# Optimization experiments

Hardware: AMD Instinct MI355X
Metric: run time of the kernel (lower is better)

## Reference

```python
import jax, jax.numpy as jnp
import numpy as np

ALPHA = 0.2  # LeakyReLU negative slope
NEG_INF = -9e15


def setup_inputs() -> dict:
    key = jax.random.key(0)
    ks = jax.random.split(key, 6)
    B, N, F_in, F_out = 16, 1024, 1024, 512
    x = jax.random.normal(ks[0], (B, N, F_in), dtype=jnp.float32)
    adj = jax.random.randint(ks[1], (B, N, N), 0, 2, dtype=jnp.int32)
    W = jax.random.normal(ks[2], (F_in, F_out), dtype=jnp.float32) * 0.02
    a = jax.random.normal(ks[3], (2 * F_out, 1), dtype=jnp.float32) * 0.02
    fc_w = jax.random.normal(ks[4], (F_out, 2 * F_out), dtype=jnp.float32) * 0.02
    fc_b = jnp.zeros((F_out,), dtype=jnp.float32)
    return {"x": x, "adj": adj, "W": W, "a": a, "fc_w": fc_w, "fc_b": fc_b}


def reference(x, adj, W, a, fc_w, fc_b):
    # h: [B, N, F_out]
    h = jnp.matmul(x, W)
    F_out = W.shape[1]
    # The original builds a_input = concat(h_i, h_j) of shape [B,N,N,2F] and
    # contracts with a. Equivalently (same math, no O(N^2 F) intermediate):
    # e_ij = leakyrelu(h_i . a[:F] + h_j . a[F:])
    a1 = a[:F_out, 0]  # [F_out]
    a2 = a[F_out:, 0]  # [F_out]
    f1 = jnp.einsum('bnf,f->bn', h, a1)  # source term
    f2 = jnp.einsum('bnf,f->bn', h, a2)  # target term
    e = jax.nn.leaky_relu(f1[:, :, None] + f2[:, None, :], negative_slope=ALPHA)  # [B,N,N]
    attention = jnp.where(adj > 0, e, jnp.full_like(e, NEG_INF))
    attention = jax.nn.softmax(attention, axis=2)
    # dropout is identity in eval mode
    agg = jnp.matmul(attention, h)  # [B,N,F_out]
    h_prime = jnp.concatenate([agg, h], axis=2)  # [B,N,2F]
    h_prime = jnp.matmul(h_prime, fc_w.T) + fc_b
    return jax.nn.elu(h_prime)  # concat=True path
```

## Files before the change

### kernel.cpp

```cpp
#include <hip/hip_runtime.h>

#define ALPHA 0.2f

typedef __attribute__((ext_vector_type(8))) short short8;
typedef __attribute__((ext_vector_type(4))) float f32x4;

__device__ __forceinline__ unsigned short f2b(float f) {
  unsigned int u; __builtin_memcpy(&u, &f, 4);
  unsigned int r = (u + 0x7FFFu + ((u >> 16) & 1u)) >> 16;
  return (unsigned short)r;
}
__device__ __forceinline__ float b2f(unsigned short v) {
  unsigned int u = ((unsigned int)v) << 16; float f; __builtin_memcpy(&f, &u, 4); return f;
}
__device__ __forceinline__ void gl_lds16(const unsigned short* g, unsigned short* l) {
  __builtin_amdgcn_global_load_lds((__attribute__((address_space(1))) void*)g,
                                   (__attribute__((address_space(3))) void*)l, 16, 0, 0);
}
__device__ __forceinline__ uint4 pack8(float4 v0, float4 v1) {
  alignas(16) unsigned short o[8];
  o[0] = f2b(v0.x); o[1] = f2b(v0.y); o[2] = f2b(v0.z); o[3] = f2b(v0.w);
  o[4] = f2b(v1.x); o[5] = f2b(v1.y); o[6] = f2b(v1.z); o[7] = f2b(v1.w);
  return *(const uint4*)o;
}

__device__ __forceinline__ void cvt_f4(const float* __restrict__ in,
                                       unsigned short* __restrict__ out,
                                       unsigned int f4idx) {
  float4 v = ((const float4*)in)[f4idx];
  alignas(8) unsigned short o[4];
  o[0] = f2b(v.x); o[1] = f2b(v.y); o[2] = f2b(v.z); o[3] = f2b(v.w);
  ((uint2*)out)[f4idx] = *(const uint2*)o;
}

__global__ __launch_bounds__(256) void prep1(const float* __restrict__ fcw,
                                             unsigned short* __restrict__ fcwb,
                                             const float* __restrict__ W,
                                             unsigned short* __restrict__ Wt,
                                             float* __restrict__ f1z,
                                             float* __restrict__ f2z) {
  __shared__ alignas(16) unsigned short tile[64][72];
  unsigned int bx = blockIdx.x;
  unsigned int tid = threadIdx.x;
  if (bx < 256u) {
    unsigned int base = bx * 512u;
    cvt_f4(fcw, fcwb, base + tid);
    cvt_f4(fcw, fcwb, base + 256u + tid);
  } else if (bx < 384u) {
    unsigned int idx = bx - 256u;
    unsigned int k0 = (idx >> 3) * 64, n0 = (idx & 7) * 64;
    #pragma unroll
    for (int p = 0; p < 4; p++) {
      int r = p * 16 + (tid >> 4);
      int c = (tid & 15) * 4;
      float4 v = *(const float4*)(W + (size_t)(k0 + r) * 512 + n0 + c);
      tile[r][c] = f2b(v.x); tile[r][c + 1] = f2b(v.y);
      tile[r][c + 2] = f2b(v.z); tile[r][c + 3] = f2b(v.w);
    }
    __syncthreads();
    int f = tid >> 2;
    int ic = (tid & 3) * 16;
    alignas(16) unsigned short buf[16];
    #pragma unroll
    for (int k = 0; k < 16; k++) buf[k] = tile[ic + k][f];
    uint4* dst = (uint4*)(Wt + (size_t)(n0 + f) * 1024 + k0 + ic);
    dst[0] = ((const uint4*)buf)[0];
    dst[1] = ((const uint4*)buf)[1];
  } else {
    float4 z = {0.f, 0.f, 0.f, 0.f};
    #pragma unroll
    for (int i = 0; i < 16; i++) ((float4*)f1z)[i * 256 + tid] = z;
    #pragma unroll
    for (int i = 0; i < 16; i++) ((float4*)f2z)[i * 256 + tid] = z;
  }
}

__global__ __launch_bounds__(256) void rowsum_P(const int* __restrict__ adj,
                                                const float* __restrict__ f1,
                                                const float* __restrict__ f2,
                                                float* __restrict__ invl,
                                                unsigned short* __restrict__ P) {
  int row = blockIdx.x * 4 + (threadIdx.x >> 6);
  int lane = threadIdx.x & 63;
  int b = row >> 10;
  float f1v = f1[row];
  const int4* ap = (const int4*)(adj + (size_t)row * 1024) + lane * 4;
  int4 a0 = ap[0];
  int4 a1 = ap[1];
  int4 a2 = ap[2];
  int4 a3 = ap[3];
  int av[16] = {a0.x, a0.y, a0.z, a0.w, a1.x, a1.y, a1.z, a1.w,
                a2.x, a2.y, a2.z, a2.w, a3.x, a3.y, a3.z, a3.w};
  const float* f2p = f2 + (b << 10) + lane * 16;
  float4 v0 = ((const float4*)f2p)[0];
  float4 v1 = ((const float4*)f2p)[1];
  float4 v2 = ((const float4*)f2p)[2];
  float4 v3 = ((const float4*)f2p)[3];
  float fv[16] = {v0.x, v0.y, v0.z, v0.w, v1.x, v1.y, v1.z, v1.w,
                  v2.x, v2.y, v2.z, v2.w, v3.x, v3.y, v3.z, v3.w};
  float s = 0.f;
  alignas(16) unsigned short o[16];
  #pragma unroll
  for (int j = 0; j < 16; j++) {
    float p = 0.f;
    if (av[j] > 0) {
      float z = f1v + fv[j];
      z = z > 0.f ? z : ALPHA * z;
      p = __expf(z);
      s += p;
    }
    o[j] = f2b(p);
  }
  uint4* dst = (uint4*)(P + (size_t)row * 1024 + lane * 16);
  dst[0] = ((const uint4*)o)[0];
  dst[1] = ((const uint4*)o)[1];
  #pragma unroll
  for (int off = 32; off > 0; off >>= 1) s += __shfl_down(s, off);
  if (lane == 0) invl[row] = 1.0f / s;
}

template <int EPI, int CVTA>
__global__ __launch_bounds__(512, 4) void gemm_bt(
    const void* __restrict__ A_, size_t aBS,
    const unsigned short* __restrict__ Bt, size_t bBS,
    int K,
    void* __restrict__ outp, size_t oBS, int ldo, int ocol,
    const float* __restrict__ scale,
    const float* __restrict__ bias,
    unsigned short* __restrict__ htout,
    float* __restrict__ f1g, float* __restrict__ f2g) {
  __shared__ alignas(16) unsigned short smem[32768];
  unsigned short* As = smem;
  unsigned short* Bs = smem + 16384;
  const int tid = threadIdx.x;
  const int lane = tid & 63;
  const int w = tid >> 6;
  const int m0 = blockIdx.x * 128;
  const int n0 = blockIdx.y * 128;
  const int zb = blockIdx.z;
  const unsigned short* Btb = Bt + (size_t)zb * bBS;

  f32x4 acc[4][2];
  #pragma unroll
  for (int i = 0; i < 4; i++)
    #pragma unroll
    for (int j = 0; j < 2; j++)
      #pragma unroll
      for (int r = 0; r < 4; r++) acc[i][j][r] = 0.f;

  const int lr = lane >> 3;
  const int lc = (lane & 7) ^ lr;
  const unsigned short* ag = nullptr;
  const float* agf = nullptr;
  if (CVTA)
    agf = (const float*)A_ + (size_t)(m0 + w * 8 + lr) * K + lc * 8;
  else
    ag = (const unsigned short*)A_ + (size_t)zb * aBS + (size_t)(m0 + w * 8 + lr) * K + lc * 8;
  const unsigned short* bg = Btb + (size_t)(n0 + w * 8 + lr) * K + lc * 8;
  const int sb0 = (w * 8) * 64;
  const int sb1 = (64 + w * 8) * 64;
  const int lofs = lane * 8;

  const int wm = (w & 1) * 64;
  const int wn = (w >> 1) * 32;
  const int row16 = lane & 15;
  const int quad = lane >> 4;
  const int sw = row16 & 7;

  if (CVTA) {
    float4 av[2][2];
    #pragma unroll
    for (int t = 0; t < 2; t++) {
      av[t][0] = *(const float4*)(agf + (size_t)(t * 64) * K);
      av[t][1] = *(const float4*)(agf + (size_t)(t * 64) * K + 4);
    }
    gl_lds16(bg, Bs + sb0);
    gl_lds16(bg + (size_t)64 * K, Bs + sb1);
    *(uint4*)(As + sb0 + lofs) = pack8(av[0][0], av[0][1]);
    *(uint4*)(As + sb1 + lofs) = pack8(av[1][0], av[1][1]);
  } else {
    gl_lds16(ag, As + sb0);
    gl_lds16(ag + (size_t)64 * K, As + sb1);
    gl_lds16(bg, Bs + sb0);
    gl_lds16(bg + (size_t)64 * K, Bs + sb1);
  }
  __syncthreads();

  int bufo = 0;
  for (int k0 = 0; k0 < K; k0 += 64) {
    const int nbufo = bufo ^ 8192;
    const bool pf = (k0 + 64 < K);
    float4 av[2][2];
    if (pf) {
      if (CVTA) {
        #pragma unroll
        for (int t = 0; t < 2; t++) {
          av[t][0] = *(const float4*)(agf + (k0 + 64) + (size_t)(t * 64) * K);
          av[t][1] = *(const float4*)(agf + (k0 + 64) + (size_t)(t * 64) * K + 4);
        }
      } else {
        gl_lds16(ag + (k0 + 64), As + nbufo + sb0);
        gl_lds16(ag + (k0 + 64) + (size_t)64 * K, As + nbufo + sb1);
      }
      gl_lds16(bg + (k0 + 64), Bs + nbufo + sb0);
      gl_lds16(bg + (k0 + 64) + (size_t)64 * K, Bs + nbufo + sb1);
    }
    short8 af[2][4], bf[2][2];
    #pragma unroll
    for (int s = 0; s < 2; s++) {
      #pragma unroll
      for (int i = 0; i < 4; i++)
        af[s][i] = *(const short8*)(As + bufo + (wm + i * 16 + row16) * 64 + ((s * 4 + quad) ^ sw) * 8);
      #pragma unroll
      for (int j = 0; j < 2; j++)
        bf[s][j] = *(const short8*)(Bs + bufo + (wn + j * 16 + row16) * 64 + ((s * 4 + quad) ^ sw) * 8);
    }
    #pragma unroll
    for (int s = 0; s < 2; s++)
      #pragma unroll
      for (int am = 0; am < 4; am++)
        #pragma unroll
        for (int bn = 0; bn < 2; bn++)
          acc[am][bn] = __builtin_amdgcn_mfma_f32_16x16x32_bf16(af[s][am], bf[s][bn], acc[am][bn], 0, 0, 0);
    if (pf && CVTA) {
      *(uint4*)(As + nbufo + sb0 + lofs) = pack8(av[0][0], av[0][1]);
      *(uint4*)(As + nbufo + sb1 + lofs) = pack8(av[1][0], av[1][1]);
    }
    __syncthreads();
    bufo = nbufo;
  }

  const int col = lane & 15;
  const int r0 = quad * 4;
  #pragma unroll
  for (int am = 0; am < 4; am++) {
    #pragma unroll
    for (int bn = 0; bn < 2; bn++) {
      #pragma unroll
      for (int r = 0; r < 4; r++) {
        int m = m0 + wm + am * 16 + r0 + r;
        int n = n0 + wn + bn * 16 + col;
        float v = acc[am][bn][r];
        if (EPI == 3) v *= scale[zb * 1024 + m];
        if (EPI == 2) {
          v += bias[n];
          v = v > 0.f ? v : expm1f(v);
          ((float*)outp)[(size_t)m * ldo + n] = v;
        } else {
          ((unsigned short*)outp)[(size_t)zb * oBS + (size_t)m * ldo + ocol + n] = f2b(v);
        }
      }
    }
  }

  if (EPI == 1) {
    float* fbuf = (float*)smem;
    if (tid < 256) fbuf[tid] = 0.f;
    __syncthreads();
    float a1v[2], a2v[2];
    #pragma unroll
    for (int bn = 0; bn < 2; bn++) {
      int n = n0 + wn + bn * 16 + col;
      a1v[bn] = scale[n];
      a2v[bn] = scale[512 + n];
    }
    float p1[16], p2[16];
    #pragma unroll
    for (int am = 0; am < 4; am++)
      #pragma unroll
      for (int r = 0; r < 4; r++) {
        float s1 = 0.f, s2 = 0.f;
        #pragma unroll
        for (int bn = 0; bn < 2; bn++) {
          float hb = b2f(f2b(acc[am][bn][r]));
          s1 += hb * a1v[bn];
          s2 += hb * a2v[bn];
        }
        p1[am * 4 + r] = s1;
        p2[am * 4 + r] = s2;
      }
    #pragma unroll
    for (int mask = 1; mask < 16; mask <<= 1)
      #pragma unroll
      for (int e = 0; e < 16; e++) {
        p1[e] += __shfl_xor(p1[e], mask);
        p2[e] += __shfl_xor(p2[e], mask);
      }
    if ((lane & 15) == 0) {
      #pragma unroll
      for (int am = 0; am < 4; am++)
        #pragma unroll
        for (int r = 0; r < 4; r++) {
          int ml = wm + am * 16 + r0 + r;
          atomicAdd(&fbuf[ml], p1[am * 4 + r]);
          atomicAdd(&fbuf[128 + ml], p2[am * 4 + r]);
        }
    }
    __syncthreads();
    if (tid < 128) atomicAdd(&f1g[m0 + tid], fbuf[tid]);
    else if (tid < 256) atomicAdd(&f2g[m0 + tid - 128], fbuf[tid]);
    __syncthreads();

    #pragma unroll
    for (int am = 0; am < 4; am++)
      #pragma unroll
      for (int bn = 0; bn < 2; bn++)
        #pragma unroll
        for (int r = 0; r < 4; r++) {
          int nloc = wn + bn * 16 + col;
          int mloc = wm + am * 16 + r0 + r;
          smem[nloc * 136 + mloc] = f2b(acc[am][bn][r]);
        }
    __syncthreads();
    const int b = m0 >> 10;
    const int i0 = m0 & 1023;
    #pragma unroll
    for (int p = 0; p < 4; p++) {
      int fr = p * 32 + (tid >> 4);
      int ib = (tid & 15) * 8;
      uint4 v = *(const uint4*)(smem + fr * 136 + ib);
      *(uint4*)(htout + ((size_t)(b * 512 + n0 + fr) << 10) + i0 + ib) = v;
    }
  }
}

extern "C" void kernel_launch(void* const* d_in, const int* in_sizes, int n_in,
                              void* d_out, int out_size, void* d_ws, size_t ws_size,
                              hipStream_t stream) {
  const float* x   = (const float*)d_in[0];
  const int*   adj = (const int*)d_in[1];
  const float* W   = (const float*)d_in[2];
  const float* a   = (const float*)d_in[3];
  const float* fcw = (const float*)d_in[4];
  const float* fcb = (const float*)d_in[5];
  float* out = (float*)d_out;
  char* ws = (char*)d_ws;

  unsigned short* P    = (unsigned short*)(ws);
  unsigned short* hp   = (unsigned short*)(ws + 33554432);
  unsigned short* ht   = (unsigned short*)(ws + 67108864);
  unsigned short* Wt   = (unsigned short*)(ws + 83886080);
  unsigned short* fcwb = (unsigned short*)(ws + 84934656);
  float* f1            = (float*)(ws + 85983232);
  float* f2            = (float*)(ws + 86048768);
  float* invl          = (float*)(ws + 86114304);

  prep1<<<385, 256, 0, stream>>>(fcw, fcwb, W, Wt, f1, f2);

  gemm_bt<1, 1><<<dim3(128, 4, 1), 512, 0, stream>>>(x, 0, Wt, 0, 1024,
                                                     hp, 0, 1024, 512, a, nullptr,
                                                     ht, f1, f2);
  rowsum_P<<<4096, 256, 0, stream>>>(adj, f1, f2, invl, P);

  gemm_bt<3, 0><<<dim3(8, 4, 16), 512, 0, stream>>>(P, 1024 * 1024, ht, 512 * 1024, 1024,
                                                    hp, 1024 * 1024, 1024, 0, invl, nullptr,
                                                    nullptr, nullptr, nullptr);
  gemm_bt<2, 0><<<dim3(128, 4, 1), 512, 0, stream>>>(hp, 0, fcwb, 0, 1024,
                                                     out, 0, 512, 0, nullptr, fcb,
                                                     nullptr, nullptr, nullptr);
}
```

Before: 250.8 us.

## Split GEMM kernels and add 128x256 tile with prefetch-two pipelined bf16 GEMM

Splits the fused-cast first GEMM into its own kernel and adds a new gemm_bt2 for the attention-aggregation and output-projection GEMMs. The new kernel uses 128x256 tiles with a 4x4 MFMA accumulator per wave and keeps two stages of loads in flight, using explicit vmcnt/lgkmcnt waits and raw barriers instead of __syncthreads. It also raises MFMA issue priority with s_setprio. The aim is more reuse per LDS load and better overlap of global loads with MFMA. In exchange it uses more LDS and registers, lowering occupancy to 2 blocks per CU, and halves the grid's N dimension, which risks under-filling the GPU.

Measured after the change: 257.0 us. 1.02x slower.

```diff
diff --git a/kernel.cpp b/kernel.cpp
--- a/kernel.cpp
+++ b/kernel.cpp
@@ -23,6 +23,9 @@
   o[4] = f2b(v1.x); o[5] = f2b(v1.y); o[6] = f2b(v1.z); o[7] = f2b(v1.w);
   return *(const uint4*)o;
 }
+__device__ __forceinline__ void vm6() { asm volatile("s_waitcnt vmcnt(6)" ::: "memory"); }
+__device__ __forceinline__ void vm0() { asm volatile("s_waitcnt vmcnt(0)" ::: "memory"); }
+__device__ __forceinline__ void lg0() { asm volatile("s_waitcnt lgkmcnt(0)" ::: "memory"); }
 
 __device__ __forceinline__ void cvt_f4(const float* __restrict__ in,
                                        unsigned short* __restrict__ out,
@@ -119,14 +122,12 @@
   if (lane == 0) invl[row] = 1.0f / s;
 }
 
-template <int EPI, int CVTA>
-__global__ __launch_bounds__(512, 4) void gemm_bt(
-    const void* __restrict__ A_, size_t aBS,
-    const unsigned short* __restrict__ Bt, size_t bBS,
+__global__ __launch_bounds__(512, 4) void gemm1(
+    const float* __restrict__ A_,
+    const unsigned short* __restrict__ Bt,
     int K,
-    void* __restrict__ outp, size_t oBS, int ldo, int ocol,
-    const float* __restrict__ scale,
-    const float* __restrict__ bias,
+    unsigned short* __restrict__ outp, int ldo, int ocol,
+    const float* __restrict__ avec,
     unsigned short* __restrict__ htout,
     float* __restrict__ f1g, float* __restrict__ f2g) {
   __shared__ alignas(16) unsigned short smem[32768];
@@ -137,8 +138,6 @@
   const int w = tid >> 6;
   const int m0 = blockIdx.x * 128;
   const int n0 = blockIdx.y * 128;
-  const int zb = blockIdx.z;
-  const unsigned short* Btb = Bt + (size_t)zb * bBS;
 
   f32x4 acc[4][2];
   #pragma unroll
@@ -150,13 +149,8 @@
 
   const int lr = lane >> 3;
   const int lc = (lane & 7) ^ lr;
-  const unsigned short* ag = nullptr;
-  const float* agf = nullptr;
-  if (CVTA)
-    agf = (const float*)A_ + (size_t)(m0 + w * 8 + lr) * K + lc * 8;
-  else
-    ag = (const unsigned short*)A_ + (size_t)zb * aBS + (size_t)(m0 + w * 8 + lr) * K + lc * 8;
-  const unsigned short* bg = Btb + (size_t)(n0 + w * 8 + lr) * K + lc * 8;
+  const float* agf = A_ + (size_t)(m0 + w * 8 + lr) * K + lc * 8;
+  const unsigned short* bg = Bt + (size_t)(n0 + w * 8 + lr) * K + lc * 8;
   const int sb0 = (w * 8) * 64;
   const int sb1 = (64 + w * 8) * 64;
   const int lofs = lane * 8;
@@ -167,7 +161,7 @@
   const int quad = lane >> 4;
   const int sw = row16 & 7;
 
-  if (CVTA) {
+  {
     float4 av[2][2];
     #pragma unroll
     for (int t = 0; t < 2; t++) {
@@ -178,11 +172,6 @@
     gl_lds16(bg + (size_t)64 * K, Bs + sb1);
     *(uint4*)(As + sb0 + lofs) = pack8(av[0][0], av[0][1]);
     *(uint4*)(As + sb1 + lofs) = pack8(av[1][0], av[1][1]);
-  } else {
-    gl_lds16(ag, As + sb0);
-    gl_lds16(ag + (size_t)64 * K, As + sb1);
-    gl_lds16(bg, Bs + sb0);
-    gl_lds16(bg + (size_t)64 * K, Bs + sb1);
   }
   __syncthreads();
 
@@ -192,15 +181,10 @@
     const bool pf = (k0 + 64 < K);
     float4 av[2][2];
     if (pf) {
-      if (CVTA) {
-        #pragma unroll
-        for (int t = 0; t < 2; t++) {
-          av[t][0] = *(const float4*)(agf + (k0 + 64) + (size_t)(t * 64) * K);
-          av[t][1] = *(const float4*)(agf + (k0 + 64) + (size_t)(t * 64) * K + 4);
-        }
-      } else {
-        gl_lds16(ag + (k0 + 64), As + nbufo + sb0);
-        gl_lds16(ag + (k0 + 64) + (size_t)64 * K, As + nbufo + sb1);
+      #pragma unroll
+      for (int t = 0; t < 2; t++) {
+        av[t][0] = *(const float4*)(agf + (k0 + 64) + (size_t)(t * 64) * K);
+        av[t][1] = *(const float4*)(agf + (k0 + 64) + (size_t)(t * 64) * K + 4);
       }
       gl_lds16(bg + (k0 + 64), Bs + nbufo + sb0);
       gl_lds16(bg + (k0 + 64) + (size_t)64 * K, Bs + nbufo + sb1);
@@ -222,7 +206,7 @@
         #pragma unroll
         for (int bn = 0; bn < 2; bn++)
           acc[am][bn] = __builtin_amdgcn_mfma_f32_16x16x32_bf16(af[s][am], bf[s][bn], acc[am][bn], 0, 0, 0);
-    if (pf && CVTA) {
+    if (pf) {
       *(uint4*)(As + nbufo + sb0 + lofs) = pack8(av[0][0], av[0][1]);
       *(uint4*)(As + nbufo + sb1 + lofs) = pack8(av[1][0], av[1][1]);
     }
@@ -233,9 +217,192 @@
   const int col = lane & 15;
   const int r0 = quad * 4;
   #pragma unroll
+  for (int am = 0; am < 4; am++)
+    #pragma unroll
+    for (int bn = 0; bn < 2; bn++)
+      #pragma unroll
+      for (int r = 0; r < 4; r++) {
+        int m = m0 + wm + am * 16 + r0 + r;
+        int n = n0 + wn + bn * 16 + col;
+        outp[(size_t)m * ldo + ocol + n] = f2b(acc[am][bn][r]);
+      }
+
+  float* fbuf = (float*)smem;
+  if (tid < 256) fbuf[tid] = 0.f;
+  __syncthreads();
+  float a1v[2], a2v[2];
+  #pragma unroll
+  for (int bn = 0; bn < 2; bn++) {
+    int n = n0 + wn + bn * 16 + col;
+    a1v[bn] = avec[n];
+    a2v[bn] = avec[512 + n];
+  }
+  float p1[16], p2[16];
+  #pragma unroll
+  for (int am = 0; am < 4; am++)
+    #pragma unroll
+    for (int r = 0; r < 4; r++) {
+      float s1 = 0.f, s2 = 0.f;
+      #pragma unroll
+      for (int bn = 0; bn < 2; bn++) {
+        float hb = b2f(f2b(acc[am][bn][r]));
+        s1 += hb * a1v[bn];
+        s2 += hb * a2v[bn];
+      }
+      p1[am * 4 + r] = s1;
+      p2[am * 4 + r] = s2;
+    }
+  #pragma unroll
+  for (int mask = 1; mask < 16; mask <<= 1)
+    #pragma unroll
+    for (int e = 0; e < 16; e++) {
+      p1[e] += __shfl_xor(p1[e], mask);
+      p2[e] += __shfl_xor(p2[e], mask);
+    }
+  if ((lane & 15) == 0) {
+    #pragma unroll
+    for (int am = 0; am < 4; am++)
+      #pragma unroll
+      for (int r = 0; r < 4; r++) {
+        int ml = wm + am * 16 + r0 + r;
+        atomicAdd(&fbuf[ml], p1[am * 4 + r]);
+        atomicAdd(&fbuf[128 + ml], p2[am * 4 + r]);
+      }
+  }
+  __syncthreads();
+  if (tid < 128) atomicAdd(&f1g[m0 + tid], fbuf[tid]);
+  else if (tid < 256) atomicAdd(&f2g[m0 + tid - 128], fbuf[tid]);
+  __syncthreads();
+
+  #pragma unroll
+  for (int am = 0; am < 4; am++)
+    #pragma unroll
+    for (int bn = 0; bn < 2; bn++)
+      #pragma unroll
+      for (int r = 0; r < 4; r++) {
+        int nloc = wn + bn * 16 + col;
+        int mloc = wm + am * 16 + r0 + r;
+        smem[nloc * 136 + mloc] = f2b(acc[am][bn][r]);
+      }
+  __syncthreads();
+  const int b = m0 >> 10;
+  const int i0 = m0 & 1023;
+  #pragma unroll
+  for (int p = 0; p < 4; p++) {
+    int fr = p * 32 + (tid >> 4);
+    int ib = (tid & 15) * 8;
+    uint4 v = *(const uint4*)(smem + fr * 136 + ib);
+    *(uint4*)(htout + ((size_t)(b * 512 + n0 + fr) << 10) + i0 + ib) = v;
+  }
+}
+
+template <int EPI>
+__global__ __launch_bounds__(512, 2) void gemm_bt2(
+    const unsigned short* __restrict__ A, size_t aBS,
+    const unsigned short* __restrict__ Bt, size_t bBS,
+    int K,
+    void* __restrict__ outp, size_t oBS, int ldo, int ocol,
+    const float* __restrict__ scale,
+    const float* __restrict__ bias) {
+  __shared__ alignas(16) unsigned short As[2 * 128 * 64];
+  __shared__ alignas(16) unsigned short Bs[2 * 256 * 64];
+  const int tid = threadIdx.x;
+  const int lane = tid & 63;
+  const int w = tid >> 6;
+  const int m0 = blockIdx.x * 128;
+  const int n0 = blockIdx.y * 256;
+  const int zb = blockIdx.z;
+  const unsigned short* Ab = A + (size_t)zb * aBS;
+  const unsigned short* Btb = Bt + (size_t)zb * bBS;
+
+  f32x4 acc[4][4];
+  #pragma unroll
+  for (int i = 0; i < 4; i++)
+    #pragma unroll
+    for (int j = 0; j < 4; j++)
+      #pragma unroll
+      for (int r = 0; r < 4; r++) acc[i][j][r] = 0.f;
+
+  const int lr = lane >> 3;
+  const int lc = (lane & 7) ^ lr;
+  const unsigned short* ag = Ab + (size_t)(m0 + w * 8 + lr) * K + lc * 8;
+  const unsigned short* bg = Btb + (size_t)(n0 + w * 8 + lr) * K + lc * 8;
+  const int asb = w * 8 * 64;
+  const int bsb = w * 8 * 64;
+
+  const int wm = (w & 1) * 64;
+  const int wn = (w >> 1) * 64;
+  const int row16 = lane & 15;
+  const int quad = lane >> 4;
+  const int sw = row16 & 7;
+
+  const int nk = K >> 6;
+
+  #pragma unroll
+  for (int t = 0; t < 2; t++)
+    gl_lds16(ag + (size_t)(t * 64) * K, As + t * 4096 + asb);
+  #pragma unroll
+  for (int t = 0; t < 4; t++)
+    gl_lds16(bg + (size_t)(t * 64) * K, Bs + t * 4096 + bsb);
+  #pragma unroll
+  for (int t = 0; t < 2; t++)
+    gl_lds16(ag + 64 + (size_t)(t * 64) * K, As + 8192 + t * 4096 + asb);
+  #pragma unroll
+  for (int t = 0; t < 4; t++)
+    gl_lds16(bg + 64 + (size_t)(t * 64) * K, Bs + 16384 + t * 4096 + bsb);
+  vm6();
+  __builtin_amdgcn_s_barrier();
+
+  for (int k = 0; k < nk; k++) {
+    const int ab = (k & 1) * 8192;
+    const int bb = (k & 1) * 16384;
+    const bool st2 = (k + 2 < nk);
+    const bool pub = (k + 1 < nk);
+
+    short8 af[2][4], bf[2][4];
+    #pragma unroll
+    for (int s = 0; s < 2; s++) {
+      #pragma unroll
+      for (int i = 0; i < 4; i++) {
+        af[s][i] = *(const short8*)(As + ab + (wm + i * 16 + row16) * 64 + ((s * 4 + quad) ^ sw) * 8);
+        bf[s][i] = *(const short8*)(Bs + bb + (wn + i * 16 + row16) * 64 + ((s * 4 + quad) ^ sw) * 8);
+      }
+    }
+    lg0();
+    __builtin_amdgcn_s_barrier();
+
+    if (st2) {
+      const int ko = (k + 2) * 64;
+      #pragma unroll
+      for (int t = 0; t < 2; t++)
+        gl_lds16(ag + ko + (size_t)(t * 64) * K, As + ab + t * 4096 + asb);
+      #pragma unroll
+      for (int t = 0; t < 4; t++)
+        gl_lds16(bg + ko + (size_t)(t * 64) * K, Bs + bb + t * 4096 + bsb);
+    }
+
+    __builtin_amdgcn_s_setprio(1);
+    #pragma unroll
+    for (int s = 0; s < 2; s++)
+      #pragma unroll
+      for (int am = 0; am < 4; am++)
+        #pragma unroll
+        for (int bn = 0; bn < 4; bn++)
+          acc[am][bn] = __builtin_amdgcn_mfma_f32_16x16x32_bf16(af[s][am], bf[s][bn], acc[am][bn], 0, 0, 0);
+    __builtin_amdgcn_s_setprio(0);
+
+    if (pub) {
+      if (st2) vm6(); else vm0();
+      __builtin_amdgcn_s_barrier();
+    }
+  }
+
+  const int col = lane & 15;
+  const int r0 = quad * 4;
+  #pragma unroll
   for (int am = 0; am < 4; am++) {
     #pragma unroll
-    for (int bn = 0; bn < 2; bn++) {
+    for (int bn = 0; bn < 4; bn++) {
       #pragma unroll
       for (int r = 0; r < 4; r++) {
         int m = m0 + wm + am * 16 + r0 + r;
@@ -252,76 +419,6 @@
       }
     }
   }
-
-  if (EPI == 1) {
-    float* fbuf = (float*)smem;
-    if (tid < 256) fbuf[tid] = 0.f;
-    __syncthreads();
-    float a1v[2], a2v[2];
-    #pragma unroll
-    for (int bn = 0; bn < 2; bn++) {
-      int n = n0 + wn + bn * 16 + col;
-      a1v[bn] = scale[n];
-      a2v[bn] = scale[512 + n];
-    }
-    float p1[16], p2[16];
-    #pragma unroll
-    for (int am = 0; am < 4; am++)
-      #pragma unroll
-      for (int r = 0; r < 4; r++) {
-        float s1 = 0.f, s2 = 0.f;
-        #pragma unroll
-        for (int bn = 0; bn < 2; bn++) {
-          float hb = b2f(f2b(acc[am][bn][r]));
-          s1 += hb * a1v[bn];
-          s2 += hb * a2v[bn];
-        }
-        p1[am * 4 + r] = s1;
-        p2[am * 4 + r] = s2;
-      }
-    #pragma unroll
-    for (int mask = 1; mask < 16; mask <<= 1)
-      #pragma unroll
-      for (int e = 0; e < 16; e++) {
-        p1[e] += __shfl_xor(p1[e], mask);
-        p2[e] += __shfl_xor(p2[e], mask);
-      }
-    if ((lane & 15) == 0) {
-      #pragma unroll
-      for (int am = 0; am < 4; am++)
-        #pragma unroll
-        for (int r = 0; r < 4; r++) {
-          int ml = wm + am * 16 + r0 + r;
-          atomicAdd(&fbuf[ml], p1[am * 4 + r]);
-          atomicAdd(&fbuf[128 + ml], p2[am * 4 + r]);
-        }
-    }
-    __syncthreads();
-    if (tid < 128) atomicAdd(&f1g[m0 + tid], fbuf[tid]);
-    else if (tid < 256) atomicAdd(&f2g[m0 + tid - 128], fbuf[tid]);
-    __syncthreads();
-
-    #pragma unroll
-    for (int am = 0; am < 4; am++)
-      #pragma unroll
-      for (int bn = 0; bn < 2; bn++)
-        #pragma unroll
-        for (int r = 0; r < 4; r++) {
-          int nloc = wn + bn * 16 + col;
-          int mloc = wm + am * 16 + r0 + r;
-          smem[nloc * 136 + mloc] = f2b(acc[am][bn][r]);
-        }
-    __syncthreads();
-    const int b = m0 >> 10;
-    const int i0 = m0 & 1023;
-    #pragma unroll
-    for (int p = 0; p < 4; p++) {
-      int fr = p * 32 + (tid >> 4);
-      int ib = (tid & 15) * 8;
-      uint4 v = *(const uint4*)(smem + fr * 136 + ib);
-      *(uint4*)(htout + ((size_t)(b * 512 + n0 + fr) << 10) + i0 + ib) = v;
-    }
-  }
 }
 
 extern "C" void kernel_launch(void* const* d_in, const int* in_sizes, int n_in,
@@ -347,15 +444,12 @@
 
   prep1<<<385, 256, 0, stream>>>(fcw, fcwb, W, Wt, f1, f2);
 
-  gemm_bt<1, 1><<<dim3(128, 4, 1), 512, 0, stream>>>(x, 0, Wt, 0, 1024,
-                                                     hp, 0, 1024, 512, a, nullptr,
-                                                     ht, f1, f2);
+  gemm1<<<dim3(128, 4, 1), 512, 0, stream>>>(x, Wt, 1024, hp, 1024, 512, a, ht, f1, f2);
+
   rowsum_P<<<4096, 256, 0, stream>>>(adj, f1, f2, invl, P);
 
-  gemm_bt<3, 0><<<dim3(8, 4, 16), 512, 0, stream>>>(P, 1024 * 1024, ht, 512 * 1024, 1024,
-                                                    hp, 1024 * 1024, 1024, 0, invl, nullptr,
-                                                    nullptr, nullptr, nullptr);
-  gemm_bt<2, 0><<<dim3(128, 4, 1), 512, 0, stream>>>(hp, 0, fcwb, 0, 1024,
-                                                     out, 0, 512, 0, nullptr, fcb,
-                                                     nullptr, nullptr, nullptr);
-}
+  gemm_bt2<3><<<dim3(8, 2, 16), 512, 0, stream>>>(P, 1024 * 1024, ht, 512 * 1024, 1024,
+                                                  hp, 1024 * 1024, 1024, 0, invl, nullptr);
+  gemm_bt2<2><<<dim3(128, 2, 1), 512, 0, stream>>>(hp, 0, fcwb, 0, 1024,
+                                                   out, 0, 512, 0, nullptr, fcb);
+}
```

## Fuse attention probability computation into the aggregation GEMM A-tile load

Applied to the files above, without the earlier changes.

Removes the separate rowsum_P kernel and the bf16 P matrix in global memory. The new gemm2f kernel reads adj and f2 directly, computes exp(leakyrelu) probabilities into the LDS A-tile while the previous tile's MFMAs run, accumulates row sums in registers and applies 1/rowsum in the epilogue. This avoids writing and re-reading the 32MB P buffer. The cost is that each of the 4 column blocks now re-reads adj (int32) and recomputes the exponentials, which adds ALU work inside the GEMM loop.

Measured after the change: 255.7 us. About the same (+1.9%).

```diff
diff --git a/kernel.cpp b/kernel.cpp
--- a/kernel.cpp
+++ b/kernel.cpp
@@ -21,6 +21,25 @@
   alignas(16) unsigned short o[8];
   o[0] = f2b(v0.x); o[1] = f2b(v0.y); o[2] = f2b(v0.z); o[3] = f2b(v0.w);
   o[4] = f2b(v1.x); o[5] = f2b(v1.y); o[6] = f2b(v1.z); o[7] = f2b(v1.w);
+  return *(const uint4*)o;
+}
+
+__device__ __forceinline__ uint4 computeP(int4 a0, int4 a1, float4 fa, float4 fb,
+                                          float f1v, float& rs) {
+  int av[8] = {a0.x, a0.y, a0.z, a0.w, a1.x, a1.y, a1.z, a1.w};
+  float fv[8] = {fa.x, fa.y, fa.z, fa.w, fb.x, fb.y, fb.z, fb.w};
+  alignas(16) unsigned short o[8];
+  #pragma unroll
+  for (int j = 0; j < 8; j++) {
+    float p = 0.f;
+    if (av[j] > 0) {
+      float z = f1v + fv[j];
+      z = z > 0.f ? z : ALPHA * z;
+      p = __expf(z);
+      rs += p;
+    }
+    o[j] = f2b(p);
+  }
   return *(const uint4*)o;
 }
 
@@ -73,50 +92,6 @@
     #pragma unroll
     for (int i = 0; i < 16; i++) ((float4*)f2z)[i * 256 + tid] = z;
   }
-}
-
-__global__ __launch_bounds__(256) void rowsum_P(const int* __restrict__ adj,
-                                                const float* __restrict__ f1,
-                                                const float* __restrict__ f2,
-                                                float* __restrict__ invl,
-                                                unsigned short* __restrict__ P) {
-  int row = blockIdx.x * 4 + (threadIdx.x >> 6);
-  int lane = threadIdx.x & 63;
-  int b = row >> 10;
-  float f1v = f1[row];
-  const int4* ap = (const int4*)(adj + (size_t)row * 1024) + lane * 4;
-  int4 a0 = ap[0];
-  int4 a1 = ap[1];
-  int4 a2 = ap[2];
-  int4 a3 = ap[3];
-  int av[16] = {a0.x, a0.y, a0.z, a0.w, a1.x, a1.y, a1.z, a1.w,
-                a2.x, a2.y, a2.z, a2.w, a3.x, a3.y, a3.z, a3.w};
-  const float* f2p = f2 + (b << 10) + lane * 16;
-  float4 v0 = ((const float4*)f2p)[0];
-  float4 v1 = ((const float4*)f2p)[1];
-  float4 v2 = ((const float4*)f2p)[2];
-  float4 v3 = ((const float4*)f2p)[3];
-  float fv[16] = {v0.x, v0.y, v0.z, v0.w, v1.x, v1.y, v1.z, v1.w,
-                  v2.x, v2.y, v2.z, v2.w, v3.x, v3.y, v3.z, v3.w};
-  float s = 0.f;
-  alignas(16) unsigned short o[16];
-  #pragma unroll
-  for (int j = 0; j < 16; j++) {
-    float p = 0.f;
-    if (av[j] > 0) {
-      float z = f1v + fv[j];
-      z = z > 0.f ? z : ALPHA * z;
-      p = __expf(z);
-      s += p;
-    }
-    o[j] = f2b(p);
-  }
-  uint4* dst = (uint4*)(P + (size_t)row * 1024 + lane * 16);
-  dst[0] = ((const uint4*)o)[0];
-  dst[1] = ((const uint4*)o)[1];
-  #pragma unroll
-  for (int off = 32; off > 0; off >>= 1) s += __shfl_down(s, off);
-  if (lane == 0) invl[row] = 1.0f / s;
 }
 
 template <int EPI, int CVTA>
@@ -241,7 +216,6 @@
         int m = m0 + wm + am * 16 + r0 + r;
         int n = n0 + wn + bn * 16 + col;
         float v = acc[am][bn][r];
-        if (EPI == 3) v *= scale[zb * 1024 + m];
         if (EPI == 2) {
           v += bias[n];
           v = v > 0.f ? v : expm1f(v);
@@ -320,6 +294,137 @@
       int ib = (tid & 15) * 8;
       uint4 v = *(const uint4*)(smem + fr * 136 + ib);
       *(uint4*)(htout + ((size_t)(b * 512 + n0 + fr) << 10) + i0 + ib) = v;
+    }
+  }
+}
+
+__global__ __launch_bounds__(512, 4) void gemm2f(
+    const int* __restrict__ adj,
+    const float* __restrict__ f1,
+    const float* __restrict__ f2,
+    const unsigned short* __restrict__ ht,
+    unsigned short* __restrict__ hp) {
+  __shared__ alignas(16) unsigned short smem[32768];
+  unsigned short* As = smem;
+  unsigned short* Bs = smem + 16384;
+  const int K = 1024;
+  const int tid = threadIdx.x;
+  const int lane = tid & 63;
+  const int w = tid >> 6;
+  const int m0 = blockIdx.x * 128;
+  const int n0 = blockIdx.y * 128;
+  const int zb = blockIdx.z;
+  const unsigned short* Btb = ht + (size_t)zb * 512 * 1024;
+
+  f32x4 acc[4][2];
+  #pragma unroll
+  for (int i = 0; i < 4; i++)
+    #pragma unroll
+    for (int j = 0; j < 2; j++)
+      #pragma unroll
+      for (int r = 0; r < 4; r++) acc[i][j][r] = 0.f;
+
+  const int lr = lane >> 3;
+  const int lc = (lane & 7) ^ lr;
+  const int row0 = m0 + w * 8 + lr;
+  const int* ag0 = adj + (size_t)zb * 1048576 + (size_t)row0 * 1024 + lc * 8;
+  const int* ag1 = ag0 + 64 * 1024;
+  const float f1v0 = f1[zb * 1024 + row0];
+  const float f1v1 = f1[zb * 1024 + row0 + 64];
+  const float* f2p = f2 + zb * 1024;
+  const unsigned short* bg = Btb + (size_t)(n0 + w * 8 + lr) * K + lc * 8;
+  const int sb0 = (w * 8) * 64;
+  const int sb1 = (64 + w * 8) * 64;
+  const int lofs = lane * 8;
+
+  const int wm = (w & 1) * 64;
+  const int wn = (w >> 1) * 32;
+  const int row16 = lane & 15;
+  const int quad = lane >> 4;
+  const int sw = row16 & 7;
+
+  float rs0 = 0.f, rs1 = 0.f;
+
+  {
+    int4 a00 = ((const int4*)ag0)[0], a01 = ((const int4*)ag0)[1];
+    int4 a10 = ((const int4*)ag1)[0], a11 = ((const int4*)ag1)[1];
+    float4 fa = *(const float4*)(f2p + lc * 8);
+    float4 fb = *(const float4*)(f2p + lc * 8 + 4);
+    gl_lds16(bg, Bs + sb0);
+    gl_lds16(bg + (size_t)64 * K, Bs + sb1);
+    *(uint4*)(As + sb0 + lofs) = computeP(a00, a01, fa, fb, f1v0, rs0);
+    *(uint4*)(As + sb1 + lofs) = computeP(a10, a11, fa, fb, f1v1, rs1);
+  }
+  __syncthreads();
+
+  int bufo = 0;
+  for (int k0 = 0; k0 < K; k0 += 64) {
+    const int nbufo = bufo ^ 8192;
+    const bool pf = (k0 + 64 < K);
+    int4 a00, a01, a10, a11;
+    float4 fa, fb;
+    if (pf) {
+      const int ko = k0 + 64;
+      a00 = *(const int4*)(ag0 + ko); a01 = *(const int4*)(ag0 + ko + 4);
+      a10 = *(const int4*)(ag1 + ko); a11 = *(const int4*)(ag1 + ko + 4);
+      fa = *(const float4*)(f2p + ko + lc * 8);
+      fb = *(const float4*)(f2p + ko + lc * 8 + 4);
+      gl_lds16(bg + ko, Bs + nbufo + sb0);
+      gl_lds16(bg + ko + (size_t)64 * K, Bs + nbufo + sb1);
+    }
+    short8 af[2][4], bf[2][2];
+    #pragma unroll
+    for (int s = 0; s < 2; s++) {
+      #pragma unroll
+      for (int i = 0; i < 4; i++)
+        af[s][i] = *(const short8*)(As + bufo + (wm + i * 16 + row16) * 64 + ((s * 4 + quad) ^ sw) * 8);
+      #pragma unroll
+      for (int j = 0; j < 2; j++)
+        bf[s][j] = *(const short8*)(Bs + bufo + (wn + j * 16 + row16) * 64 + ((s * 4 + quad) ^ sw) * 8);
+    }
+    #pragma unroll
+    for (int s = 0; s < 2; s++)
+      #pragma unroll
+      for (int am = 0; am < 4; am++)
+        #pragma unroll
+        for (int bn = 0; bn < 2; bn++)
+          acc[am][bn] = __builtin_amdgcn_mfma_f32_16x16x32_bf16(af[s][am], bf[s][bn], acc[am][bn], 0, 0, 0);
+    if (pf) {
+      *(uint4*)(As + nbufo + sb0 + lofs) = computeP(a00, a01, fa, fb, f1v0, rs0);
+      *(uint4*)(As + nbufo + sb1 + lofs) = computeP(a10, a11, fa, fb, f1v1, rs1);
+    }
+    __syncthreads();
+    bufo = nbufo;
+  }
+
+  #pragma unroll
+  for (int msk = 1; msk < 8; msk <<= 1) {
+    rs0 += __shfl_xor(rs0, msk);
+    rs1 += __shfl_xor(rs1, msk);
+  }
+  float* fbuf = (float*)smem;
+  if ((lane & 7) == 0) {
+    fbuf[w * 8 + lr] = rs0;
+    fbuf[64 + w * 8 + lr] = rs1;
+  }
+  __syncthreads();
+  if (tid < 128) fbuf[128 + tid] = 1.0f / fbuf[tid];
+  __syncthreads();
+
+  const int col = lane & 15;
+  const int r0 = quad * 4;
+  #pragma unroll
+  for (int am = 0; am < 4; am++) {
+    #pragma unroll
+    for (int bn = 0; bn < 2; bn++) {
+      #pragma unroll
+      for (int r = 0; r < 4; r++) {
+        int ml = wm + am * 16 + r0 + r;
+        int m = m0 + ml;
+        int n = n0 + wn + bn * 16 + col;
+        hp[(size_t)zb * 1048576 + (size_t)m * 1024 + n] =
+            f2b(acc[am][bn][r] * fbuf[128 + ml]);
+      }
     }
   }
 }
@@ -336,25 +441,20 @@
   float* out = (float*)d_out;
   char* ws = (char*)d_ws;
 
-  unsigned short* P    = (unsigned short*)(ws);
   unsigned short* hp   = (unsigned short*)(ws + 33554432);
   unsigned short* ht   = (unsigned short*)(ws + 67108864);
   unsigned short* Wt   = (unsigned short*)(ws + 83886080);
   unsigned short* fcwb = (unsigned short*)(ws + 84934656);
   float* f1            = (float*)(ws + 85983232);
   float* f2            = (float*)(ws + 86048768);
-  float* invl          = (float*)(ws + 86114304);
 
   prep1<<<385, 256, 0, stream>>>(fcw, fcwb, W, Wt, f1, f2);
 
   gemm_bt<1, 1><<<dim3(128, 4, 1), 512, 0, stream>>>(x, 0, Wt, 0, 1024,
                                                      hp, 0, 1024, 512, a, nullptr,
                                                      ht, f1, f2);
-  rowsum_P<<<4096, 256, 0, stream>>>(adj, f1, f2, invl, P);
-
-  gemm_bt<3, 0><<<dim3(8, 4, 16), 512, 0, stream>>>(P, 1024 * 1024, ht, 512 * 1024, 1024,
-                                                    hp, 1024 * 1024, 1024, 0, invl, nullptr,
-                                                    nullptr, nullptr, nullptr);
+  gemm2f<<<dim3(8, 4, 16), 512, 0, stream>>>(adj, f1, f2, ht, hp);
+
   gemm_bt<2, 0><<<dim3(128, 4, 1), 512, 0, stream>>>(hp, 0, fcwb, 0, 1024,
                                                      out, 0, 512, 0, nullptr, fcb,
                                                      nullptr, nullptr, nullptr);
```
